# Performance work log

Measured on AMD Instinct MI355X. Metric: run time of the kernel, lower is better.

Reference implementation:

```python
import jax, jax.numpy as jnp
import numpy as np

N = 50000  # num_nodes
K_DIFF = 2  # max_diffusion_step


def _spmm(rows, cols, vals, x):
    # sparse (N,N) @ dense (N,F): y[r] += v * x[c]
    return jax.ops.segment_sum(vals[:, None] * x[cols], rows, num_segments=N)


def setup_inputs() -> dict:
    key = jax.random.key(0)
    ks = jax.random.split(key, 9)
    B, D, O, E = 8, 64, 64, 1600000
    num_matrices = 2 * K_DIFF + 1
    return {
        "x": jax.random.normal(ks[0], (B, N, D), dtype=jnp.float32),
        "rows0": jax.random.randint(ks[1], (E,), 0, N),
        "cols0": jax.random.randint(ks[2], (E,), 0, N),
        "vals0": jax.random.uniform(ks[3], (E,), dtype=jnp.float32),
        "rows1": jax.random.randint(ks[4], (E,), 0, N),
        "cols1": jax.random.randint(ks[5], (E,), 0, N),
        "vals1": jax.random.uniform(ks[6], (E,), dtype=jnp.float32),
        "weight": jax.random.normal(ks[7], (D * num_matrices, O), dtype=jnp.float32) * 0.1,
        "biases": jnp.zeros((O,), dtype=jnp.float32),
    }


def reference(x, rows0, cols0, vals0, rows1, cols1, vals1, weight, biases):
    B, n, D = x.shape
    # 'b n d -> n (b d)'
    x0 = jnp.transpose(x, (1, 0, 2)).reshape(n, B * D)
    xs = [x0]
    for (r, c, v) in ((rows0, cols0, vals0), (rows1, cols1, vals1)):
        x1 = _spmm(r, c, v, x0)
        xs.append(x1)
        x_prev, x_curr = x0, x1
        for _ in range(2, K_DIFF + 1):
            x_next = 2.0 * _spmm(r, c, v, x_curr) - x_prev
            xs.append(x_next)
            x_prev, x_curr = x_curr, x_next
    Km = len(xs)
    xk = jnp.stack(xs, axis=0).reshape(Km, n, B, D)  # k n b d
    # 'k n (b d) -> b n d k' then '(b n)(d k)'
    feat = jnp.transpose(xk, (2, 1, 3, 0)).reshape(B * n, D * Km)
    out = feat @ weight + biases
    return out.reshape(B, n, -1)
```

## Files before the change

kernel.cpp:

```cpp
#include <hip/hip_runtime.h>

#define N_NODES 50000
#define BDIM 8
#define DDIM 64
#define ODIM 64
#define KM 5
#define BD 512
#define CAP 80

typedef unsigned int u32;
typedef unsigned short u16;

typedef __attribute__((ext_vector_type(8))) short short8;
typedef __attribute__((ext_vector_type(4))) float f32x4;

__device__ __forceinline__ u16 pack1(float f) {
  u32 a = __float_as_uint(f);
  return (u16)((a + 0x7FFFu + ((a >> 16) & 1u)) >> 16);
}
__device__ __forceinline__ u32 pack2(float f0, float f1) {
  return (u32)pack1(f0) | ((u32)pack1(f1) << 16);
}
__device__ __forceinline__ float bfl(u32 u) { return __uint_as_float(u << 16); }
__device__ __forceinline__ float bfh(u32 u) { return __uint_as_float(u & 0xFFFF0000u); }

__global__ void k_transpose_h(const float* __restrict__ x, u16* __restrict__ x0h, int tot4) {
  int i = blockIdx.x * blockDim.x + threadIdx.x;
  if (i >= tot4) return;
  int f = i << 2;
  int d = f & (DDIM - 1);
  int nb = f >> 6;
  int b = nb / N_NODES;
  int n = nb - b * N_NODES;
  float4 v = *(const float4*)(x + (size_t)f);
  uint2 w = make_uint2(pack2(v.x, v.y), pack2(v.z, v.w));
  *(uint2*)(x0h + (size_t)n * BD + b * DDIM + d) = w;
}

__global__ void k_scatter_cap(const int* __restrict__ r0, const int* __restrict__ c0, const float* __restrict__ v0,
                              const int* __restrict__ r1, const int* __restrict__ c1, const float* __restrict__ v1,
                              int* __restrict__ cnt , u32* __restrict__ cv , int E4) {
  int i = blockIdx.x * blockDim.x + threadIdx.x;
  const int* rr; const int* cc; const float* vv; int base, j;
  if (i < E4) { rr = r0; cc = c0; vv = v0; base = 0; j = i; }
  else if (i < 2 * E4) { rr = r1; cc = c1; vv = v1; base = N_NODES; j = i - E4; }
  else return;
  int4 r = *(const int4*)(rr + (size_t)j * 4);
  int4 c = *(const int4*)(cc + (size_t)j * 4);
  float4 v = *(const float4*)(vv + (size_t)j * 4);
  int p;
  p = atomicAdd(&cnt[base + r.x], 1);
  if (p < CAP) cv[(size_t)(base + r.x) * CAP + p] = (u32)c.x | ((u32)pack1(v.x) << 16);
  p = atomicAdd(&cnt[base + r.y], 1);
  if (p < CAP) cv[(size_t)(base + r.y) * CAP + p] = (u32)c.y | ((u32)pack1(v.y) << 16);
  p = atomicAdd(&cnt[base + r.z], 1);
  if (p < CAP) cv[(size_t)(base + r.z) * CAP + p] = (u32)c.z | ((u32)pack1(v.z) << 16);
  p = atomicAdd(&cnt[base + r.w], 1);
  if (p < CAP) cv[(size_t)(base + r.w) * CAP + p] = (u32)c.w | ((u32)pack1(v.w) << 16);
}

__device__ __forceinline__ void fma8(float a[8], uint4 q, float v) {
  a[0] = fmaf(v, bfl(q.x), a[0]); a[1] = fmaf(v, bfh(q.x), a[1]);
  a[2] = fmaf(v, bfl(q.y), a[2]); a[3] = fmaf(v, bfh(q.y), a[3]);
  a[4] = fmaf(v, bfl(q.z), a[4]); a[5] = fmaf(v, bfh(q.z), a[5]);
  a[6] = fmaf(v, bfl(q.w), a[6]); a[7] = fmaf(v, bfh(q.w), a[7]);
}

template<bool CHEB>
__global__ void __launch_bounds__(256) k_gath(const int* __restrict__ cnt,
                                              const u32* __restrict__ cv,
                                              const u16* __restrict__ xsrc,
                                              const u16* __restrict__ x0h,
                                              u16* __restrict__ xdst) {
  int wid = threadIdx.x >> 6, lane = threadIdx.x & 63;
  int r = blockIdx.x * 4 + wid;
  int n = cnt[r];
  const u32* ecv = cv + (size_t)r * CAP;
  const u16* xb = xsrc + lane * 8;
  float A0[8] = {}, A1[8] = {}, A2[8] = {}, A3[8] = {};
  int e = 0;
  for (; e + 4 <= n; e += 4) {
    uint4 q = *(const uint4*)(ecv + e);
    uint4 d0 = *(const uint4*)(xb + (size_t)(q.x & 0xFFFFu) * BD);
    uint4 d1 = *(const uint4*)(xb + (size_t)(q.y & 0xFFFFu) * BD);
    uint4 d2 = *(const uint4*)(xb + (size_t)(q.z & 0xFFFFu) * BD);
    uint4 d3 = *(const uint4*)(xb + (size_t)(q.w & 0xFFFFu) * BD);
    fma8(A0, d0, bfh(q.x));
    fma8(A1, d1, bfh(q.y));
    fma8(A2, d2, bfh(q.z));
    fma8(A3, d3, bfh(q.w));
  }
  for (; e < n; ++e) {
    u32 q = ecv[e];
    uint4 d = *(const uint4*)(xb + (size_t)(q & 0xFFFFu) * BD);
    fma8(A0, d, bfh(q));
  }
  float acc[8];
  #pragma unroll
  for (int j = 0; j < 8; ++j) acc[j] = (A0[j] + A1[j]) + (A2[j] + A3[j]);
  if (CHEB) {
    uint4 qp = *(const uint4*)(x0h + (size_t)r * BD + lane * 8);
    float p[8] = {bfl(qp.x), bfh(qp.x), bfl(qp.y), bfh(qp.y),
                  bfl(qp.z), bfh(qp.z), bfl(qp.w), bfh(qp.w)};
    #pragma unroll
    for (int j = 0; j < 8; ++j) acc[j] = 2.f * acc[j] - p[j];
  }
  uint4 s = make_uint4(pack2(acc[0], acc[1]), pack2(acc[2], acc[3]),
                       pack2(acc[4], acc[5]), pack2(acc[6], acc[7]));
  *(uint4*)(xdst + (size_t)r * BD + lane * 8) = s;
}

__global__ void k_prep_w(const float* __restrict__ weight, u16* __restrict__ wfrag) {
  for (int i = threadIdx.x; i < 2560; i += 256) {
    int lane = i & 63;
    int ob = (i >> 6) & 3;
    int half = (i >> 8) & 1;
    int k = i >> 9;
    int o = ob * 16 + (lane & 15);
    #pragma unroll
    for (int j = 0; j < 8; ++j) {
      int d = half * 32 + ((lane >> 4) * 8) + j;
      wfrag[(size_t)i * 8 + j] = pack1(weight[(d * KM + k) * ODIM + o]);
    }
  }
}

template<int KC, int K0, bool FIRST>
__global__ void __launch_bounds__(256) k_gemm(const u16* __restrict__ s0,
                                              const u16* __restrict__ s1,
                                              const u16* __restrict__ s2,
                                              const u16* __restrict__ wfrag,
                                              const float* __restrict__ bias,
                                              float* __restrict__ out) {
  int wid = threadIdx.x >> 6, lane = threadIdx.x & 63;
  int gid = blockIdx.x * 4 + wid;
  int m0 = gid * 16;
  int b = m0 / N_NODES;
  int n0 = m0 - b * N_NODES;
  int row = lane & 15, kg = lane >> 4;
  size_t abase = (size_t)(n0 + row) * BD + b * DDIM + kg * 8;
  const u16* const sl[3] = {s0, s1, s2};
  f32x4 acc[4] = {};
  #pragma unroll
  for (int kc = 0; kc < KC; ++kc) {
    const u16* sp = sl[kc >> 1];
    short8 a = *reinterpret_cast<const short8*>(sp + abase + (kc & 1) * 32);
    const u16* wp = wfrag + ((size_t)((K0 + (kc >> 1)) * 2 + (kc & 1)) * 4) * 512 + lane * 8;
    #pragma unroll
    for (int ob = 0; ob < 4; ++ob) {
      short8 bf = *reinterpret_cast<const short8*>(wp + ob * 512);
      acc[ob] = __builtin_amdgcn_mfma_f32_16x16x32_bf16(a, bf, acc[ob], 0, 0, 0);
    }
  }
  int col = lane & 15;
  #pragma unroll
  for (int ob = 0; ob < 4; ++ob) {
    float bv = FIRST ? bias[ob * 16 + col] : 0.f;
    #pragma unroll
    for (int rg = 0; rg < 4; ++rg) {
      size_t oidx = (size_t)(m0 + kg * 4 + rg) * ODIM + ob * 16 + col;
      if (FIRST) out[oidx] = acc[ob][rg] + bv;
      else out[oidx] += acc[ob][rg];
    }
  }
}

extern "C" void kernel_launch(void* const* d_in, const int* in_sizes, int n_in,
                              void* d_out, int out_size, void* d_ws, size_t ws_size,
                              hipStream_t stream) {
  const float* x      = (const float*)d_in[0];
  const int*   rows0  = (const int*)d_in[1];
  const int*   cols0  = (const int*)d_in[2];
  const float* vals0  = (const float*)d_in[3];
  const int*   rows1  = (const int*)d_in[4];
  const int*   cols1  = (const int*)d_in[5];
  const float* vals1  = (const float*)d_in[6];
  const float* weight = (const float*)d_in[7];
  const float* bias   = (const float*)d_in[8];
  float* out = (float*)d_out;
  const int E = in_sizes[1];
  const int E4 = E >> 2;

  char* p = (char*)d_ws;
  auto alloc = [&](size_t bytes) {
    char* q = p;
    p += (bytes + 255) & ~(size_t)255;
    return q;
  };
  u16* x0h    = (u16*)alloc((size_t)N_NODES * BD * sizeof(u16));
  u16* slabA  = (u16*)alloc((size_t)N_NODES * BD * sizeof(u16));
  u16* slabB  = (u16*)alloc((size_t)N_NODES * BD * sizeof(u16));
  int* cnt    = (int*)alloc((size_t)2 * N_NODES * sizeof(int));
  u32* cv     = (u32*)alloc((size_t)2 * N_NODES * CAP * sizeof(u32));
  u16* wfrag  = (u16*)alloc((size_t)2560 * 8 * sizeof(u16));
  if ((size_t)(p - (char*)d_ws) > ws_size) return;

  const int tot4 = BDIM * N_NODES * DDIM / 4;
  k_transpose_h<<<(tot4 + 255) / 256, 256, 0, stream>>>(x, x0h, tot4);

  hipMemsetAsync(cnt, 0, (size_t)2 * N_NODES * sizeof(int), stream);
  k_scatter_cap<<<(2 * E4 + 255) / 256, 256, 0, stream>>>(rows0, cols0, vals0,
                                                          rows1, cols1, vals1,
                                                          cnt, cv, E4);
  k_prep_w<<<1, 256, 0, stream>>>(weight, wfrag);

  const int GBLK = N_NODES / 4;
  const int MBLK = (BDIM * N_NODES / 16) / 4;

  k_gath<false><<<GBLK, 256, 0, stream>>>(cnt, cv, x0h, nullptr, slabA);
  k_gath<true><<<GBLK, 256, 0, stream>>>(cnt, cv, slabA, x0h, slabB);
  k_gemm<6, 0, true><<<MBLK, 256, 0, stream>>>(x0h, slabA, slabB, wfrag, bias, out);

  k_gath<false><<<GBLK, 256, 0, stream>>>(cnt + N_NODES, cv + (size_t)N_NODES * CAP,
                                          x0h, nullptr, slabA);
  k_gath<true><<<GBLK, 256, 0, stream>>>(cnt + N_NODES, cv + (size_t)N_NODES * CAP,
                                         slabA, x0h, slabB);
  k_gemm<4, 3, false><<<MBLK, 256, 0, stream>>>(slabA, slabB, nullptr, wfrag, bias, out);
}
```

Baseline: 1.234 ms.

## Degree-sort rows and slice features in SpMM gather; chunk scatter by row range

The CSR-like scatter now runs in eight row-range passes. Each pass re-reads all edges but only does the atomics whose row falls in its range, which is meant to improve atomic and write locality. New histogram, scan and permutation kernels sort rows by degree, so rows of similar length share a wavefront. The gather kernel is restructured so each 8-lane group handles one row over a 32-feature slice, with the 16 slices split into two phases of the grid, and loops to the wave's max degree. This aims to improve L2 reuse of source rows across blocks and reduce divergence. In exchange it reads the edge lists 8 times during scatter and reads each row's cv list 16 times during gather.

Result: slower. 1.946 ms (+57.7%).

```diff
diff --git a/kernel.cpp b/kernel.cpp
--- a/kernel.cpp
+++ b/kernel.cpp
@@ -7,6 +7,13 @@
 #define KM 5
 #define BD 512
 #define CAP 80
+#define SCHUNKS 8
+#define CROWS (N_NODES / SCHUNKS)
+#define SLICES 16
+#define SFEAT 32
+#define RPW 8
+#define RPB 32
+#define RBLK 1563
 
 typedef unsigned int u32;
 typedef unsigned short u16;
@@ -37,10 +44,13 @@
   *(uint2*)(x0h + (size_t)n * BD + b * DDIM + d) = w;
 }
 
-__global__ void k_scatter_cap(const int* __restrict__ r0, const int* __restrict__ c0, const float* __restrict__ v0,
-                              const int* __restrict__ r1, const int* __restrict__ c1, const float* __restrict__ v1,
-                              int* __restrict__ cnt , u32* __restrict__ cv , int E4) {
-  int i = blockIdx.x * blockDim.x + threadIdx.x;
+__global__ void __launch_bounds__(256) k_scatter_cap(
+    const int* __restrict__ r0, const int* __restrict__ c0, const float* __restrict__ v0,
+    const int* __restrict__ r1, const int* __restrict__ c1, const float* __restrict__ v1,
+    int* __restrict__ cnt , u32* __restrict__ cv , int E4, int bpc) {
+  int chunk = blockIdx.x / bpc;
+  int i = (blockIdx.x - chunk * bpc) * blockDim.x + threadIdx.x;
+  int lo = chunk * CROWS;
   const int* rr; const int* cc; const float* vv; int base, j;
   if (i < E4) { rr = r0; cc = c0; vv = v0; base = 0; j = i; }
   else if (i < 2 * E4) { rr = r1; cc = c1; vv = v1; base = N_NODES; j = i - E4; }
@@ -49,65 +59,103 @@
   int4 c = *(const int4*)(cc + (size_t)j * 4);
   float4 v = *(const float4*)(vv + (size_t)j * 4);
   int p;
-  p = atomicAdd(&cnt[base + r.x], 1);
-  if (p < CAP) cv[(size_t)(base + r.x) * CAP + p] = (u32)c.x | ((u32)pack1(v.x) << 16);
-  p = atomicAdd(&cnt[base + r.y], 1);
-  if (p < CAP) cv[(size_t)(base + r.y) * CAP + p] = (u32)c.y | ((u32)pack1(v.y) << 16);
-  p = atomicAdd(&cnt[base + r.z], 1);
-  if (p < CAP) cv[(size_t)(base + r.z) * CAP + p] = (u32)c.z | ((u32)pack1(v.z) << 16);
-  p = atomicAdd(&cnt[base + r.w], 1);
-  if (p < CAP) cv[(size_t)(base + r.w) * CAP + p] = (u32)c.w | ((u32)pack1(v.w) << 16);
-}
-
-__device__ __forceinline__ void fma8(float a[8], uint4 q, float v) {
-  a[0] = fmaf(v, bfl(q.x), a[0]); a[1] = fmaf(v, bfh(q.x), a[1]);
-  a[2] = fmaf(v, bfl(q.y), a[2]); a[3] = fmaf(v, bfh(q.y), a[3]);
-  a[4] = fmaf(v, bfl(q.z), a[4]); a[5] = fmaf(v, bfh(q.z), a[5]);
-  a[6] = fmaf(v, bfl(q.w), a[6]); a[7] = fmaf(v, bfh(q.w), a[7]);
+  if ((u32)(r.x - lo) < CROWS) {
+    p = atomicAdd(&cnt[base + r.x], 1);
+    if (p < CAP) cv[(size_t)(base + r.x) * CAP + p] = (u32)c.x | ((u32)pack1(v.x) << 16);
+  }
+  if ((u32)(r.y - lo) < CROWS) {
+    p = atomicAdd(&cnt[base + r.y], 1);
+    if (p < CAP) cv[(size_t)(base + r.y) * CAP + p] = (u32)c.y | ((u32)pack1(v.y) << 16);
+  }
+  if ((u32)(r.z - lo) < CROWS) {
+    p = atomicAdd(&cnt[base + r.z], 1);
+    if (p < CAP) cv[(size_t)(base + r.z) * CAP + p] = (u32)c.z | ((u32)pack1(v.z) << 16);
+  }
+  if ((u32)(r.w - lo) < CROWS) {
+    p = atomicAdd(&cnt[base + r.w], 1);
+    if (p < CAP) cv[(size_t)(base + r.w) * CAP + p] = (u32)c.w | ((u32)pack1(v.w) << 16);
+  }
+}
+
+__global__ void k_deghist(const int* __restrict__ cnt, int* __restrict__ bins ) {
+  int i = blockIdx.x * blockDim.x + threadIdx.x;
+  if (i >= 2 * N_NODES) return;
+  int g = i >= N_NODES;
+  int d = min(cnt[i], CAP);
+  atomicAdd(&bins[g * (CAP + 1) + d], 1);
+}
+
+__global__ void k_degscan(const int* __restrict__ bins, int* __restrict__ cur) {
+  __shared__ int lb[2 * (CAP + 1)];
+  int t = threadIdx.x;
+  if (t < 2 * (CAP + 1)) lb[t] = bins[t];
+  __syncthreads();
+  if (t < 2 * (CAP + 1)) {
+    int g = t / (CAP + 1);
+    int d = t - g * (CAP + 1);
+    int run = 0;
+    for (int i = 0; i < d; ++i) run += lb[g * (CAP + 1) + i];
+    cur[t] = run;
+  }
+}
+
+__global__ void k_permscat(const int* __restrict__ cnt, int* __restrict__ cur,
+                           int* __restrict__ perm ) {
+  int i = blockIdx.x * blockDim.x + threadIdx.x;
+  if (i >= 2 * N_NODES) return;
+  int g = i >= N_NODES;
+  int r = g ? i - N_NODES : i;
+  int d = min(cnt[i], CAP);
+  int p = atomicAdd(&cur[g * (CAP + 1) + d], 1);
+  perm[g * N_NODES + p] = r;
 }
 
 template<bool CHEB>
 __global__ void __launch_bounds__(256) k_gath(const int* __restrict__ cnt,
                                               const u32* __restrict__ cv,
+                                              const int* __restrict__ perm,
                                               const u16* __restrict__ xsrc,
                                               const u16* __restrict__ x0h,
                                               u16* __restrict__ xdst) {
+  int bid = blockIdx.x;
+  int phase = bid / (8 * RBLK);
+  int rem = bid - phase * (8 * RBLK);
+  int rb = rem >> 3;
+  int s = (rem & 7) + 8 * phase;
   int wid = threadIdx.x >> 6, lane = threadIdx.x & 63;
-  int r = blockIdx.x * 4 + wid;
-  int n = cnt[r];
+  int g = lane >> 3;
+  int pe = lane & 7;
+  int ridx = rb * RPB + wid * RPW + g;
+  bool rvalid = ridx < N_NODES;
+  int r = rvalid ? perm[ridx] : 0;
+  int n = rvalid ? min(cnt[r], CAP) : 0;
+  int nmax = n;
+  #pragma unroll
+  for (int off = 1; off < 64; off <<= 1)
+    nmax = max(nmax, __shfl_xor(nmax, off));
   const u32* ecv = cv + (size_t)r * CAP;
-  const u16* xb = xsrc + lane * 8;
-  float A0[8] = {}, A1[8] = {}, A2[8] = {}, A3[8] = {};
-  int e = 0;
-  for (; e + 4 <= n; e += 4) {
-    uint4 q = *(const uint4*)(ecv + e);
-    uint4 d0 = *(const uint4*)(xb + (size_t)(q.x & 0xFFFFu) * BD);
-    uint4 d1 = *(const uint4*)(xb + (size_t)(q.y & 0xFFFFu) * BD);
-    uint4 d2 = *(const uint4*)(xb + (size_t)(q.z & 0xFFFFu) * BD);
-    uint4 d3 = *(const uint4*)(xb + (size_t)(q.w & 0xFFFFu) * BD);
-    fma8(A0, d0, bfh(q.x));
-    fma8(A1, d1, bfh(q.y));
-    fma8(A2, d2, bfh(q.z));
-    fma8(A3, d3, bfh(q.w));
-  }
-  for (; e < n; ++e) {
-    u32 q = ecv[e];
-    uint4 d = *(const uint4*)(xb + (size_t)(q & 0xFFFFu) * BD);
-    fma8(A0, d, bfh(q));
-  }
-  float acc[8];
-  #pragma unroll
-  for (int j = 0; j < 8; ++j) acc[j] = (A0[j] + A1[j]) + (A2[j] + A3[j]);
+  const u16* xb = xsrc + s * SFEAT + pe * 4;
+  float a0 = 0.f, a1 = 0.f, a2 = 0.f, a3 = 0.f;
+  u32 q = (nmax > 0) ? ecv[0] : 0;
+  for (int e = 0; e < nmax; ++e) {
+    u32 qc = q;
+    if (e + 1 < nmax) q = ecv[e + 1];
+    float v = __uint_as_float(qc & 0xFFFF0000u);
+    v = (e < n) ? v : 0.f;
+    uint2 d = *(const uint2*)(xb + (size_t)(qc & 0xFFFFu) * BD);
+    a0 = fmaf(v, bfl(d.x), a0);
+    a1 = fmaf(v, bfh(d.x), a1);
+    a2 = fmaf(v, bfl(d.y), a2);
+    a3 = fmaf(v, bfh(d.y), a3);
+  }
+  size_t doff = (size_t)r * BD + s * SFEAT + pe * 4;
   if (CHEB) {
-    uint4 qp = *(const uint4*)(x0h + (size_t)r * BD + lane * 8);
-    float p[8] = {bfl(qp.x), bfh(qp.x), bfl(qp.y), bfh(qp.y),
-                  bfl(qp.z), bfh(qp.z), bfl(qp.w), bfh(qp.w)};
-    #pragma unroll
-    for (int j = 0; j < 8; ++j) acc[j] = 2.f * acc[j] - p[j];
-  }
-  uint4 s = make_uint4(pack2(acc[0], acc[1]), pack2(acc[2], acc[3]),
-                       pack2(acc[4], acc[5]), pack2(acc[6], acc[7]));
-  *(uint4*)(xdst + (size_t)r * BD + lane * 8) = s;
+    uint2 p = *(const uint2*)(x0h + doff);
+    a0 = 2.f * a0 - bfl(p.x); a1 = 2.f * a1 - bfh(p.x);
+    a2 = 2.f * a2 - bfl(p.y); a3 = 2.f * a3 - bfh(p.y);
+  }
+  if (rvalid)
+    *(uint2*)(xdst + doff) = make_uint2(pack2(a0, a1), pack2(a2, a3));
 }
 
 __global__ void k_prep_w(const float* __restrict__ weight, u16* __restrict__ wfrag) {
@@ -192,6 +240,9 @@
   u16* slabB  = (u16*)alloc((size_t)N_NODES * BD * sizeof(u16));
   int* cnt    = (int*)alloc((size_t)2 * N_NODES * sizeof(int));
   u32* cv     = (u32*)alloc((size_t)2 * N_NODES * CAP * sizeof(u32));
+  int* perm   = (int*)alloc((size_t)2 * N_NODES * sizeof(int));
+  int* bins   = (int*)alloc((size_t)2 * (CAP + 1) * sizeof(int));
+  int* cur    = (int*)alloc((size_t)2 * (CAP + 1) * sizeof(int));
   u16* wfrag  = (u16*)alloc((size_t)2560 * 8 * sizeof(u16));
   if ((size_t)(p - (char*)d_ws) > ws_size) return;
 
@@ -199,21 +250,26 @@
   k_transpose_h<<<(tot4 + 255) / 256, 256, 0, stream>>>(x, x0h, tot4);
 
   hipMemsetAsync(cnt, 0, (size_t)2 * N_NODES * sizeof(int), stream);
-  k_scatter_cap<<<(2 * E4 + 255) / 256, 256, 0, stream>>>(rows0, cols0, vals0,
-                                                          rows1, cols1, vals1,
-                                                          cnt, cv, E4);
+  hipMemsetAsync(bins, 0, (size_t)2 * (CAP + 1) * sizeof(int), stream);
+  const int bpc = (2 * E4 + 255) / 256;
+  k_scatter_cap<<<SCHUNKS * bpc, 256, 0, stream>>>(rows0, cols0, vals0,
+                                                   rows1, cols1, vals1,
+                                                   cnt, cv, E4, bpc);
+  k_deghist<<<(2 * N_NODES + 255) / 256, 256, 0, stream>>>(cnt, bins);
+  k_degscan<<<1, 256, 0, stream>>>(bins, cur);
+  k_permscat<<<(2 * N_NODES + 255) / 256, 256, 0, stream>>>(cnt, cur, perm);
   k_prep_w<<<1, 256, 0, stream>>>(weight, wfrag);
 
-  const int GBLK = N_NODES / 4;
+  const int GBLK = 2 * 8 * RBLK;
   const int MBLK = (BDIM * N_NODES / 16) / 4;
 
-  k_gath<false><<<GBLK, 256, 0, stream>>>(cnt, cv, x0h, nullptr, slabA);
-  k_gath<true><<<GBLK, 256, 0, stream>>>(cnt, cv, slabA, x0h, slabB);
+  k_gath<false><<<GBLK, 256, 0, stream>>>(cnt, cv, perm, x0h, nullptr, slabA);
+  k_gath<true><<<GBLK, 256, 0, stream>>>(cnt, cv, perm, slabA, x0h, slabB);
   k_gemm<6, 0, true><<<MBLK, 256, 0, stream>>>(x0h, slabA, slabB, wfrag, bias, out);
 
   k_gath<false><<<GBLK, 256, 0, stream>>>(cnt + N_NODES, cv + (size_t)N_NODES * CAP,
-                                          x0h, nullptr, slabA);
+                                          perm + N_NODES, x0h, nullptr, slabA);
   k_gath<true><<<GBLK, 256, 0, stream>>>(cnt + N_NODES, cv + (size_t)N_NODES * CAP,
-                                         slabA, x0h, slabB);
+                                         perm + N_NODES, slabA, x0h, slabB);
   k_gemm<4, 3, false><<<MBLK, 256, 0, stream>>>(slabA, slabB, nullptr, wfrag, bias, out);
 }
```
